# Kernel optimization log

Measured on AMD Instinct MI355X. Metric: run time of the kernel, lower is better.

The kernel has to match this reference:

```python
import jax, jax.numpy as jnp
import numpy as np
from jax import lax

B, E, V, T = 16384, 256, 128, 16
TAU = 1.0


def _gru(x, h, Wih, Whh, bih, bhh):
    # torch.nn.GRUCell math
    gi = x @ Wih.T + bih
    gh = h @ Whh.T + bhh
    ir, iz, i_n = jnp.split(gi, 3, axis=-1)
    hr, hz, h_n = jnp.split(gh, 3, axis=-1)
    r = jax.nn.sigmoid(ir + hr)
    z = jax.nn.sigmoid(iz + hz)
    n = jnp.tanh(i_n + r * h_n)
    return (1.0 - z) * n + z * h


def setup_inputs() -> dict:
    key = jax.random.key(0)
    ks = jax.random.split(key, 10)
    s = 0.05
    w = lambda k, shape: jax.random.normal(k, shape, jnp.float32) * s
    return {
        "x": jax.random.normal(ks[0], (B, E), jnp.float32),
        "global_idxes": jnp.arange(B, dtype=jnp.int32),
        "uniform_noise": jax.random.uniform(ks[1], (T, B, V), dtype=jnp.float32),
        "dec_Wd2e": w(ks[2], (E, V)), "dec_bd2e": jnp.zeros((E,), jnp.float32),
        "dec_Wih": w(ks[3], (3 * E, E)), "dec_Whh": w(ks[4], (3 * E, E)),
        "dec_bih": jnp.zeros((3 * E,), jnp.float32), "dec_bhh": jnp.zeros((3 * E,), jnp.float32),
        "dec_We2d": w(ks[5], (V, E)), "dec_be2d": jnp.zeros((V,), jnp.float32),
        "enc_Wd2e": w(ks[6], (E, V)), "enc_bd2e": jnp.zeros((E,), jnp.float32),
        "enc_Wih": w(ks[7], (3 * E, E)), "enc_Whh": w(ks[8], (3 * E, E)),
        "enc_bih": jnp.zeros((3 * E,), jnp.float32), "enc_bhh": jnp.zeros((3 * E,), jnp.float32),
    }


def _forward(x, uniform_noise,
             dec_Wd2e, dec_bd2e, dec_Wih, dec_Whh, dec_bih, dec_bhh, dec_We2d, dec_be2d,
             enc_Wd2e, enc_bd2e, enc_Wih, enc_Whh, enc_bih, enc_bhh):
    Bn = x.shape[0]
    # gumbel noise from pre-sampled uniforms (deterministic)
    gnoise = -jnp.log(-jnp.log(uniform_noise + 1e-10) + 1e-10)  # [T,B,V]

    # ---- GumbelDecoder: sequential GRUCell decode with alive/dead masking ----
    def dec_step(carry, g_t):
        state, last_tok, alive, N, t = carry
        emb = last_tok @ dec_Wd2e.T + dec_bd2e
        state = _gru(emb, state, dec_Wih, dec_Whh, dec_bih, dec_bhh)
        logits = state @ dec_We2d.T + dec_be2d
        y_soft = jax.nn.softmax((logits + g_t) / TAU, axis=-1)
        idx = jnp.argmax(y_soft, axis=-1)
        y_hard = jax.nn.one_hot(idx, V, dtype=y_soft.dtype)
        # straight-through hard gumbel-softmax
        y = y_soft + lax.stop_gradient(y_hard - y_soft)
        ended = idx == 0  # token 0 is the terminator
        N = jnp.where(ended, jnp.minimum(N, t), N)
        alive = alive & (~ended)
        # dead rows (incl. newly ended) have their token zeroed, as in torch
        y = jnp.where(alive[:, None], y, 0.0)
        return (state, y, alive, N, t + 1), y

    init = (x, jnp.zeros((Bn, V), x.dtype), jnp.ones((Bn,), bool),
            jnp.full((Bn,), T, jnp.int32), jnp.int32(0))
    (_, _, _, N, _), utt = lax.scan(dec_step, init, gnoise)  # utt: [T,B,V]

    # ---- OnehotEncoder: sequential GRUCell encode with alive sieve (masked) ----
    def enc_step(carry, u_t):
        state, out_state, alive = carry
        emb = u_t @ enc_Wd2e.T + enc_bd2e
        state = _gru(emb, state, enc_Wih, enc_Whh, enc_bih, enc_bhh)
        out_state = jnp.where(alive[:, None], state, out_state)
        ended = u_t[:, 0] > 0.5  # terminator seen in utterance
        alive = alive & (~ended)
        return (state, out_state, alive), None

    z0 = jnp.zeros((Bn, E), x.dtype)
    (_, reconst, _), _ = lax.scan(enc_step, (z0, z0, jnp.ones((Bn,), bool)), utt)

    utterance = jnp.transpose(utt, (1, 0, 2))  # [B,T,V]
    return utterance, N, reconst


def reference(x, global_idxes, uniform_noise,
              dec_Wd2e, dec_bd2e, dec_Wih, dec_Whh, dec_bih, dec_bhh, dec_We2d, dec_be2d,
              enc_Wd2e, enc_bd2e, enc_Wih, enc_Whh, enc_bih, enc_bhh):
    del global_idxes  # unused by the original forward
    return _forward(x, uniform_noise,
                    dec_Wd2e, dec_bd2e, dec_Wih, dec_Whh, dec_bih, dec_bhh, dec_We2d, dec_be2d,
                    enc_Wd2e, enc_bd2e, enc_Wih, enc_Whh, enc_bih, enc_bhh)
```

## Files before the change

kernel.cpp:

```cpp
#include <hip/hip_runtime.h>


namespace {
constexpr int kB  = 16384;
constexpr int kE  = 256;
constexpr int kV  = 128;
constexpr int kT  = 16;
constexpr int kG3 = 768;
constexpr int kR  = 16;

constexpr int kOffWdhhT  = 0;
constexpr int kOffWehhT  = kG3 * kE;
constexpr int kOffWe2dT  = 2 * kG3 * kE;
constexpr int kOffDecTab = kOffWe2dT + kV * kE;
constexpr int kOffEncTab = kOffDecTab + 129 * kG3;
}

__device__ __forceinline__ float sigmf(float v) { return 1.0f / (1.0f + expf(-v)); }
__device__ __forceinline__ float gumbelf(float u) {
  return -logf(-logf(u + 1e-10f) + 1e-10f);
}

__global__ void prep_transpose(const float* __restrict__ dWhh,
                               const float* __restrict__ eWhh,
                               const float* __restrict__ We2d,
                               float* __restrict__ ws) {
  const int n1 = kG3 * kE;
  const int n2 = n1 + kG3 * kE;
  const int n3 = n2 + kV * kE;
  for (int i = blockIdx.x * blockDim.x + threadIdx.x; i < n3;
       i += gridDim.x * blockDim.x) {
    if (i < n1) {
      const int k = i / kG3, j = i - k * kG3;
      ws[i] = dWhh[j * kE + k];
    } else if (i < n2) {
      const int t = i - n1;
      const int k = t / kG3, j = t - k * kG3;
      ws[i] = eWhh[j * kE + k];
    } else {
      const int t = i - n2;
      const int k = t / kV, v = t - k * kV;
      ws[i] = We2d[v * kE + k];
    }
  }
}

__global__ void prep_tables(const float* __restrict__ Wih,
                            const float* __restrict__ Wd2e,
                            const float* __restrict__ bd2e,
                            const float* __restrict__ bih,
                            float* __restrict__ tab) {
  const int i = blockIdx.x * blockDim.x + threadIdx.x;
  if (i >= 129 * kG3) return;
  const int v = i / kG3, j = i - v * kG3;
  const float* wr = Wih + j * kE;
  float acc = 0.0f;
  if (v < kV) {
    for (int k = 0; k < kE; ++k) acc = fmaf(wr[k], Wd2e[k * kV + v] + bd2e[k], acc);
  } else {
    for (int k = 0; k < kE; ++k) acc = fmaf(wr[k], bd2e[k], acc);
  }
  tab[i] = acc + bih[j];
}

__device__ __forceinline__ void mv16(float acc[kR][3], const float (*h)[kR],
                                     const float* __restrict__ WT, const int u) {
#pragma unroll
  for (int r = 0; r < kR; ++r) { acc[r][0] = 0.f; acc[r][1] = 0.f; acc[r][2] = 0.f; }
  const float* wp = WT + u;
#pragma unroll 2
  for (int k = 0; k < kE; ++k) {
    const float4 hA = *(const float4*)(&h[k][0]);
    const float4 hB = *(const float4*)(&h[k][4]);
    const float4 hC = *(const float4*)(&h[k][8]);
    const float4 hD = *(const float4*)(&h[k][12]);
    const float w0 = wp[0], w1 = wp[kE], w2 = wp[2 * kE];
    wp += kG3;
    const float hv[kR] = {hA.x, hA.y, hA.z, hA.w, hB.x, hB.y, hB.z, hB.w,
                          hC.x, hC.y, hC.z, hC.w, hD.x, hD.y, hD.z, hD.w};
#pragma unroll
    for (int r = 0; r < kR; ++r) {
      acc[r][0] = fmaf(hv[r], w0, acc[r][0]);
      acc[r][1] = fmaf(hv[r], w1, acc[r][1]);
      acc[r][2] = fmaf(hv[r], w2, acc[r][2]);
    }
  }
}

__device__ __forceinline__ void pw16(const float acc[kR][3], float (*h)[kR],
                                     const float* __restrict__ Tab,
                                     const int* toks,
                                     const float br, const float bz,
                                     const float bn, const int u) {
  const float4 o0 = *(const float4*)(&h[u][0]);
  const float4 o1 = *(const float4*)(&h[u][4]);
  const float4 o2 = *(const float4*)(&h[u][8]);
  const float4 o3 = *(const float4*)(&h[u][12]);
  const float ho[kR] = {o0.x, o0.y, o0.z, o0.w, o1.x, o1.y, o1.z, o1.w,
                        o2.x, o2.y, o2.z, o2.w, o3.x, o3.y, o3.z, o3.w};
  float hn[kR];
#pragma unroll
  for (int r = 0; r < kR; ++r) {
    const float* gp = Tab + toks[r] * kG3 + u;
    const float gr = gp[0], gz = gp[kE], gn = gp[2 * kE];
    const float rg = sigmf(gr + acc[r][0] + br);
    const float zg = sigmf(gz + acc[r][1] + bz);
    const float ng = tanhf(gn + rg * (acc[r][2] + bn));
    hn[r] = (1.0f - zg) * ng + zg * ho[r];
  }
  *(float4*)(&h[u][0])  = make_float4(hn[0], hn[1], hn[2], hn[3]);
  *(float4*)(&h[u][4])  = make_float4(hn[4], hn[5], hn[6], hn[7]);
  *(float4*)(&h[u][8])  = make_float4(hn[8], hn[9], hn[10], hn[11]);
  *(float4*)(&h[u][12]) = make_float4(hn[12], hn[13], hn[14], hn[15]);
}

__launch_bounds__(256, 4)
__global__ void gumbel_fused(const float* __restrict__ x,
                             const float* __restrict__ unoise,
                             const float* __restrict__ dbhh,
                             const float* __restrict__ dbe2d,
                             const float* __restrict__ ebhh,
                             const float* __restrict__ ws,
                             float* __restrict__ out) {
  const float* WdhhT  = ws + kOffWdhhT;
  const float* WehhT  = ws + kOffWehhT;
  const float* We2dT  = ws + kOffWe2dT;
  const float* DecTab = ws + kOffDecTab;
  const float* EncTab = ws + kOffEncTab;

  __shared__ float hd[kE][kR];
  __shared__ float he[kE][kR];
  __shared__ int   tok_sh[kR];

  const int tid  = (int)threadIdx.x;
  const int w    = tid >> 6;
  const int jx   = tid & 63;
  const int row0 = (int)blockIdx.x * kR;
  const int u    = tid;

  for (int i = tid; i < kR * kE; i += 256) {
    const int r = i >> 8, k = i & (kE - 1);
    hd[k][r] = x[(size_t)(row0 + r) * kE + k];
    he[k][r] = 0.0f;
  }
  if (tid < kR) tok_sh[tid] = kV;
  __syncthreads();

  float Nn[4];
  bool alive[4];
#pragma unroll
  for (int q = 0; q < 4; ++q) { Nn[q] = (float)kT; alive[q] = true; }

  const float dbr = dbhh[u], dbz = dbhh[kE + u], dbn = dbhh[2 * kE + u];
  const float ebr = ebhh[u], ebz = ebhh[kE + u], ebn = ebhh[2 * kE + u];
  const float2 be2 = *(const float2*)(dbe2d + 2 * jx);

  float acc[kR][3];

  for (int t = 0; t < kT; ++t) {
    mv16(acc, hd, WdhhT, u);
    __syncthreads();
    pw16(acc, hd, DecTab, tok_sh, dbr, dbz, dbn, u);
    __syncthreads();

    mv16(acc, he, WehhT, u);

    {
      float l0[4] = {0.f, 0.f, 0.f, 0.f}, l1[4] = {0.f, 0.f, 0.f, 0.f};
      const float* wp2 = We2dT + 2 * jx;
#pragma unroll 2
      for (int k = 0; k < kE; ++k) {
        const float2 wv = *(const float2*)wp2;
        wp2 += kV;
        const float4 hq = *(const float4*)(&hd[k][4 * w]);
        const float hv[4] = {hq.x, hq.y, hq.z, hq.w};
#pragma unroll
        for (int q = 0; q < 4; ++q) {
          l0[q] = fmaf(hv[q], wv.x, l0[q]);
          l1[q] = fmaf(hv[q], wv.y, l1[q]);
        }
      }
      const size_t rbase = (size_t)row0 + 4 * w;
#pragma unroll
      for (int q = 0; q < 4; ++q) {
        const float2 uu =
            *(const float2*)(unoise + ((size_t)t * kB + rbase + q) * kV + 2 * jx);
        const float a0 = l0[q] + be2.x + gumbelf(uu.x);
        const float a1 = l1[q] + be2.y + gumbelf(uu.y);
        float mv; int mi;
        if (a1 > a0) { mv = a1; mi = 2 * jx + 1; } else { mv = a0; mi = 2 * jx; }
#pragma unroll
        for (int off = 32; off >= 1; off >>= 1) {
          const float ov = __shfl_xor(mv, off, 64);
          const int   oi = __shfl_xor(mi, off, 64);
          if (ov > mv || (ov == mv && oi < mi)) { mv = ov; mi = oi; }
        }
        const bool ended = (mi == 0);
        if (ended) Nn[q] = fminf(Nn[q], (float)t);
        const bool anew = alive[q] && !ended;
        alive[q] = anew;
        if (jx == 0) tok_sh[4 * w + q] = anew ? mi : kV;
        float2 pr;
        pr.x = (anew && mi == 2 * jx) ? 1.0f : 0.0f;
        pr.y = (anew && mi == 2 * jx + 1) ? 1.0f : 0.0f;
        *reinterpret_cast<float2*>(out + ((rbase + q) * kT + t) * kV + 2 * jx) = pr;
      }
    }
    __syncthreads();
    pw16(acc, he, EncTab, tok_sh, ebr, ebz, ebn, u);
    __syncthreads();
  }

  const size_t uttN = (size_t)kB * kT * kV;
  if (jx == 0) {
#pragma unroll
    for (int q = 0; q < 4; ++q) out[uttN + row0 + 4 * w + q] = Nn[q];
  }
  for (int i = tid; i < kR * kE; i += 256) {
    const int r = i >> 8, k = i & (kE - 1);
    out[uttN + kB + (size_t)(row0 + r) * kE + k] = he[k][r];
  }
}

extern "C" void kernel_launch(void* const* d_in, const int* in_sizes, int n_in,
                              void* d_out, int out_size, void* d_ws, size_t ws_size,
                              hipStream_t stream) {
  (void)in_sizes; (void)n_in; (void)out_size; (void)ws_size;
  const float* x      = (const float*)d_in[0];
  const float* unoise = (const float*)d_in[2];
  const float* dWd2e  = (const float*)d_in[3];
  const float* dbd2e  = (const float*)d_in[4];
  const float* dWih   = (const float*)d_in[5];
  const float* dWhh   = (const float*)d_in[6];
  const float* dbih   = (const float*)d_in[7];
  const float* dbhh   = (const float*)d_in[8];
  const float* dWe2d  = (const float*)d_in[9];
  const float* dbe2d  = (const float*)d_in[10];
  const float* eWd2e  = (const float*)d_in[11];
  const float* ebd2e  = (const float*)d_in[12];
  const float* eWih   = (const float*)d_in[13];
  const float* eWhh   = (const float*)d_in[14];
  const float* ebih   = (const float*)d_in[15];
  const float* ebhh   = (const float*)d_in[16];
  float* ws = (float*)d_ws;

  prep_transpose<<<1664, 256, 0, stream>>>(dWhh, eWhh, dWe2d, ws);
  prep_tables<<<(129 * kG3 + 255) / 256, 256, 0, stream>>>(
      dWih, dWd2e, dbd2e, dbih, ws + kOffDecTab);
  prep_tables<<<(129 * kG3 + 255) / 256, 256, 0, stream>>>(
      eWih, eWd2e, ebd2e, ebih, ws + kOffEncTab);
  gumbel_fused<<<kB / kR, 256, 0, stream>>>(
      x, unoise, dbhh, dbe2d, ebhh, ws, (float*)d_out);
}
```

Measured before the change: 4.151 ms.

## Split fused decode/encode into separate kernels with 64-row blocks and token workspace

Splits the single fused decoder+encoder kernel into a decoder kernel and an encoder kernel that communicate through a per-timestep token array in workspace. Each block now processes 64 rows with 1024 threads, and each thread computes 16 hidden units for one row using float4 weight loads and a scalar h read from LDS. This gives more reuse of each weight load across rows. The r/z parts of bhh are folded into the precomputed input tables. The changes add an extra kernel launch and global token traffic, and raise LDS use per block (64 KB) and register pressure from 48 accumulators, which may limit occupancy.

```diff
diff --git a/kernel.cpp b/kernel.cpp
--- a/kernel.cpp
+++ b/kernel.cpp
@@ -7,13 +7,13 @@
 constexpr int kV  = 128;
 constexpr int kT  = 16;
 constexpr int kG3 = 768;
-constexpr int kR  = 16;
 
 constexpr int kOffWdhhT  = 0;
 constexpr int kOffWehhT  = kG3 * kE;
 constexpr int kOffWe2dT  = 2 * kG3 * kE;
 constexpr int kOffDecTab = kOffWe2dT + kV * kE;
 constexpr int kOffEncTab = kOffDecTab + 129 * kG3;
+constexpr int kOffTok    = kOffEncTab + 129 * kG3;
 }
 
 __device__ __forceinline__ float sigmf(float v) { return 1.0f / (1.0f + expf(-v)); }
@@ -49,6 +49,7 @@
                             const float* __restrict__ Wd2e,
                             const float* __restrict__ bd2e,
                             const float* __restrict__ bih,
+                            const float* __restrict__ bhh,
                             float* __restrict__ tab) {
   const int i = blockIdx.x * blockDim.x + threadIdx.x;
   if (i >= 129 * kG3) return;
@@ -60,154 +61,143 @@
   } else {
     for (int k = 0; k < kE; ++k) acc = fmaf(wr[k], bd2e[k], acc);
   }
-  tab[i] = acc + bih[j];
-}
-
-__device__ __forceinline__ void mv16(float acc[kR][3], const float (*h)[kR],
-                                     const float* __restrict__ WT, const int u) {
-#pragma unroll
-  for (int r = 0; r < kR; ++r) { acc[r][0] = 0.f; acc[r][1] = 0.f; acc[r][2] = 0.f; }
-  const float* wp = WT + u;
-#pragma unroll 2
+  tab[i] = acc + bih[j] + (j < 2 * kE ? bhh[j] : 0.0f);
+}
+
+__device__ __forceinline__ void mv64(float acc[16][3],
+                                     const float* __restrict__ hbuf,
+                                     const float* __restrict__ WT,
+                                     const int u0, const int jx) {
+#pragma unroll
+  for (int j = 0; j < 16; ++j) { acc[j][0] = 0.f; acc[j][1] = 0.f; acc[j][2] = 0.f; }
+  const float* wk = WT + u0;
   for (int k = 0; k < kE; ++k) {
-    const float4 hA = *(const float4*)(&h[k][0]);
-    const float4 hB = *(const float4*)(&h[k][4]);
-    const float4 hC = *(const float4*)(&h[k][8]);
-    const float4 hD = *(const float4*)(&h[k][12]);
-    const float w0 = wp[0], w1 = wp[kE], w2 = wp[2 * kE];
-    wp += kG3;
-    const float hv[kR] = {hA.x, hA.y, hA.z, hA.w, hB.x, hB.y, hB.z, hB.w,
-                          hC.x, hC.y, hC.z, hC.w, hD.x, hD.y, hD.z, hD.w};
-#pragma unroll
-    for (int r = 0; r < kR; ++r) {
-      acc[r][0] = fmaf(hv[r], w0, acc[r][0]);
-      acc[r][1] = fmaf(hv[r], w1, acc[r][1]);
-      acc[r][2] = fmaf(hv[r], w2, acc[r][2]);
-    }
-  }
-}
-
-__device__ __forceinline__ void pw16(const float acc[kR][3], float (*h)[kR],
+    const float hk = hbuf[k * 64 + jx];
+    const float4 a0 = *(const float4*)(wk + 0);
+    const float4 a1 = *(const float4*)(wk + 4);
+    const float4 a2 = *(const float4*)(wk + 8);
+    const float4 a3 = *(const float4*)(wk + 12);
+    const float4 b0 = *(const float4*)(wk + kE + 0);
+    const float4 b1 = *(const float4*)(wk + kE + 4);
+    const float4 b2 = *(const float4*)(wk + kE + 8);
+    const float4 b3 = *(const float4*)(wk + kE + 12);
+    const float4 c0 = *(const float4*)(wk + 2 * kE + 0);
+    const float4 c1 = *(const float4*)(wk + 2 * kE + 4);
+    const float4 c2 = *(const float4*)(wk + 2 * kE + 8);
+    const float4 c3 = *(const float4*)(wk + 2 * kE + 12);
+    const float wa[16] = {a0.x, a0.y, a0.z, a0.w, a1.x, a1.y, a1.z, a1.w,
+                          a2.x, a2.y, a2.z, a2.w, a3.x, a3.y, a3.z, a3.w};
+    const float wb[16] = {b0.x, b0.y, b0.z, b0.w, b1.x, b1.y, b1.z, b1.w,
+                          b2.x, b2.y, b2.z, b2.w, b3.x, b3.y, b3.z, b3.w};
+    const float wc[16] = {c0.x, c0.y, c0.z, c0.w, c1.x, c1.y, c1.z, c1.w,
+                          c2.x, c2.y, c2.z, c2.w, c3.x, c3.y, c3.z, c3.w};
+#pragma unroll
+    for (int j = 0; j < 16; ++j) {
+      acc[j][0] = fmaf(hk, wa[j], acc[j][0]);
+      acc[j][1] = fmaf(hk, wb[j], acc[j][1]);
+      acc[j][2] = fmaf(hk, wc[j], acc[j][2]);
+    }
+    wk += kG3;
+  }
+}
+
+__device__ __forceinline__ void pw64(const float acc[16][3],
+                                     float* __restrict__ hbuf,
                                      const float* __restrict__ Tab,
-                                     const int* toks,
-                                     const float br, const float bz,
-                                     const float bn, const int u) {
-  const float4 o0 = *(const float4*)(&h[u][0]);
-  const float4 o1 = *(const float4*)(&h[u][4]);
-  const float4 o2 = *(const float4*)(&h[u][8]);
-  const float4 o3 = *(const float4*)(&h[u][12]);
-  const float ho[kR] = {o0.x, o0.y, o0.z, o0.w, o1.x, o1.y, o1.z, o1.w,
-                        o2.x, o2.y, o2.z, o2.w, o3.x, o3.y, o3.z, o3.w};
-  float hn[kR];
-#pragma unroll
-  for (int r = 0; r < kR; ++r) {
-    const float* gp = Tab + toks[r] * kG3 + u;
-    const float gr = gp[0], gz = gp[kE], gn = gp[2 * kE];
-    const float rg = sigmf(gr + acc[r][0] + br);
-    const float zg = sigmf(gz + acc[r][1] + bz);
-    const float ng = tanhf(gn + rg * (acc[r][2] + bn));
-    hn[r] = (1.0f - zg) * ng + zg * ho[r];
-  }
-  *(float4*)(&h[u][0])  = make_float4(hn[0], hn[1], hn[2], hn[3]);
-  *(float4*)(&h[u][4])  = make_float4(hn[4], hn[5], hn[6], hn[7]);
-  *(float4*)(&h[u][8])  = make_float4(hn[8], hn[9], hn[10], hn[11]);
-  *(float4*)(&h[u][12]) = make_float4(hn[12], hn[13], hn[14], hn[15]);
-}
-
-__launch_bounds__(256, 4)
-__global__ void gumbel_fused(const float* __restrict__ x,
-                             const float* __restrict__ unoise,
-                             const float* __restrict__ dbhh,
-                             const float* __restrict__ dbe2d,
-                             const float* __restrict__ ebhh,
-                             const float* __restrict__ ws,
-                             float* __restrict__ out) {
-  const float* WdhhT  = ws + kOffWdhhT;
-  const float* WehhT  = ws + kOffWehhT;
-  const float* We2dT  = ws + kOffWe2dT;
-  const float* DecTab = ws + kOffDecTab;
-  const float* EncTab = ws + kOffEncTab;
-
-  __shared__ float hd[kE][kR];
-  __shared__ float he[kE][kR];
-  __shared__ int   tok_sh[kR];
+                                     const float* __restrict__ bhh,
+                                     const int tk, const int u0, const int jx) {
+  const float* gp = Tab + tk * kG3 + u0;
+#pragma unroll
+  for (int j = 0; j < 16; ++j) {
+    const float gr = gp[j], gz = gp[kE + j], gn = gp[2 * kE + j];
+    const float bn = bhh[2 * kE + u0 + j];
+    const float ho = hbuf[(u0 + j) * 64 + jx];
+    const float rg = sigmf(gr + acc[j][0]);
+    const float zg = sigmf(gz + acc[j][1]);
+    const float ng = tanhf(gn + rg * (acc[j][2] + bn));
+    hbuf[(u0 + j) * 64 + jx] = (1.0f - zg) * ng + zg * ho;
+  }
+}
+
+__launch_bounds__(1024, 4)
+__global__ void dec_kernel(const float* __restrict__ x,
+                           const float* __restrict__ unoise,
+                           const float* __restrict__ dbhh,
+                           const float* __restrict__ dbe2d,
+                           const float* __restrict__ ws,
+                           int* __restrict__ tokws,
+                           float* __restrict__ out) {
+  const float* WT  = ws + kOffWdhhT;
+  const float* W2T = ws + kOffWe2dT;
+  const float* Tab = ws + kOffDecTab;
+  __shared__ float hd[kE * 64];
 
   const int tid  = (int)threadIdx.x;
   const int w    = tid >> 6;
   const int jx   = tid & 63;
-  const int row0 = (int)blockIdx.x * kR;
-  const int u    = tid;
-
-  for (int i = tid; i < kR * kE; i += 256) {
+  const int row0 = (int)blockIdx.x * 64;
+  const int u0   = __builtin_amdgcn_readfirstlane(w * 16);
+
+  for (int i = tid; i < 64 * kE; i += 1024) {
     const int r = i >> 8, k = i & (kE - 1);
-    hd[k][r] = x[(size_t)(row0 + r) * kE + k];
-    he[k][r] = 0.0f;
-  }
-  if (tid < kR) tok_sh[tid] = kV;
+    hd[k * 64 + r] = x[(size_t)(row0 + r) * kE + k];
+  }
+  if (tid < 64) tokws[row0 + tid] = kV;
   __syncthreads();
 
   float Nn[4];
   bool alive[4];
 #pragma unroll
   for (int q = 0; q < 4; ++q) { Nn[q] = (float)kT; alive[q] = true; }
-
-  const float dbr = dbhh[u], dbz = dbhh[kE + u], dbn = dbhh[2 * kE + u];
-  const float ebr = ebhh[u], ebz = ebhh[kE + u], ebn = ebhh[2 * kE + u];
   const float2 be2 = *(const float2*)(dbe2d + 2 * jx);
 
-  float acc[kR][3];
-
+  float acc[16][3];
   for (int t = 0; t < kT; ++t) {
-    mv16(acc, hd, WdhhT, u);
-    __syncthreads();
-    pw16(acc, hd, DecTab, tok_sh, dbr, dbz, dbn, u);
-    __syncthreads();
-
-    mv16(acc, he, WehhT, u);
-
-    {
-      float l0[4] = {0.f, 0.f, 0.f, 0.f}, l1[4] = {0.f, 0.f, 0.f, 0.f};
-      const float* wp2 = We2dT + 2 * jx;
+    mv64(acc, hd, WT, u0, jx);
+    __syncthreads();
+    const int tk = tokws[t * kB + row0 + jx];
+    pw64(acc, hd, Tab, dbhh, tk, u0, jx);
+    __syncthreads();
+
+    float l0[4] = {0.f, 0.f, 0.f, 0.f}, l1[4] = {0.f, 0.f, 0.f, 0.f};
+    const float* wp2 = W2T + 2 * jx;
 #pragma unroll 2
-      for (int k = 0; k < kE; ++k) {
-        const float2 wv = *(const float2*)wp2;
-        wp2 += kV;
-        const float4 hq = *(const float4*)(&hd[k][4 * w]);
-        const float hv[4] = {hq.x, hq.y, hq.z, hq.w};
-#pragma unroll
-        for (int q = 0; q < 4; ++q) {
-          l0[q] = fmaf(hv[q], wv.x, l0[q]);
-          l1[q] = fmaf(hv[q], wv.y, l1[q]);
-        }
+    for (int k = 0; k < kE; ++k) {
+      const float4 hq = *(const float4*)(&hd[k * 64 + 4 * w]);
+      const float2 wv = *(const float2*)wp2;
+      wp2 += kV;
+      const float hv[4] = {hq.x, hq.y, hq.z, hq.w};
+#pragma unroll
+      for (int q = 0; q < 4; ++q) {
+        l0[q] = fmaf(hv[q], wv.x, l0[q]);
+        l1[q] = fmaf(hv[q], wv.y, l1[q]);
       }
-      const size_t rbase = (size_t)row0 + 4 * w;
-#pragma unroll
-      for (int q = 0; q < 4; ++q) {
-        const float2 uu =
-            *(const float2*)(unoise + ((size_t)t * kB + rbase + q) * kV + 2 * jx);
-        const float a0 = l0[q] + be2.x + gumbelf(uu.x);
-        const float a1 = l1[q] + be2.y + gumbelf(uu.y);
-        float mv; int mi;
-        if (a1 > a0) { mv = a1; mi = 2 * jx + 1; } else { mv = a0; mi = 2 * jx; }
-#pragma unroll
-        for (int off = 32; off >= 1; off >>= 1) {
-          const float ov = __shfl_xor(mv, off, 64);
-          const int   oi = __shfl_xor(mi, off, 64);
-          if (ov > mv || (ov == mv && oi < mi)) { mv = ov; mi = oi; }
-        }
-        const bool ended = (mi == 0);
-        if (ended) Nn[q] = fminf(Nn[q], (float)t);
-        const bool anew = alive[q] && !ended;
-        alive[q] = anew;
-        if (jx == 0) tok_sh[4 * w + q] = anew ? mi : kV;
-        float2 pr;
-        pr.x = (anew && mi == 2 * jx) ? 1.0f : 0.0f;
-        pr.y = (anew && mi == 2 * jx + 1) ? 1.0f : 0.0f;
-        *reinterpret_cast<float2*>(out + ((rbase + q) * kT + t) * kV + 2 * jx) = pr;
+    }
+    const size_t rbase = (size_t)row0 + 4 * w;
+#pragma unroll
+    for (int q = 0; q < 4; ++q) {
+      const float2 uu =
+          *(const float2*)(unoise + ((size_t)t * kB + rbase + q) * kV + 2 * jx);
+      const float a0 = l0[q] + be2.x + gumbelf(uu.x);
+      const float a1 = l1[q] + be2.y + gumbelf(uu.y);
+      float mv; int mi;
+      if (a1 > a0) { mv = a1; mi = 2 * jx + 1; } else { mv = a0; mi = 2 * jx; }
+#pragma unroll
+      for (int off = 32; off >= 1; off >>= 1) {
+        const float ov = __shfl_xor(mv, off, 64);
+        const int   oi = __shfl_xor(mi, off, 64);
+        if (ov > mv || (ov == mv && oi < mi)) { mv = ov; mi = oi; }
       }
-    }
-    __syncthreads();
-    pw16(acc, he, EncTab, tok_sh, ebr, ebz, ebn, u);
+      const bool ended = (mi == 0);
+      if (ended) Nn[q] = fminf(Nn[q], (float)t);
+      const bool anew = alive[q] && !ended;
+      alive[q] = anew;
+      if (jx == 0) tokws[(t + 1) * kB + rbase + q] = anew ? mi : kV;
+      float2 pr;
+      pr.x = (anew && mi == 2 * jx) ? 1.0f : 0.0f;
+      pr.y = (anew && mi == 2 * jx + 1) ? 1.0f : 0.0f;
+      *reinterpret_cast<float2*>(out + ((rbase + q) * kT + t) * kV + 2 * jx) = pr;
+    }
     __syncthreads();
   }
 
@@ -216,9 +206,39 @@
 #pragma unroll
     for (int q = 0; q < 4; ++q) out[uttN + row0 + 4 * w + q] = Nn[q];
   }
-  for (int i = tid; i < kR * kE; i += 256) {
+}
+
+__launch_bounds__(1024, 4)
+__global__ void enc_kernel(const float* __restrict__ ebhh,
+                           const float* __restrict__ ws,
+                           const int* __restrict__ tokws,
+                           float* __restrict__ out) {
+  const float* WT  = ws + kOffWehhT;
+  const float* Tab = ws + kOffEncTab;
+  __shared__ float he[kE * 64];
+
+  const int tid  = (int)threadIdx.x;
+  const int w    = tid >> 6;
+  const int jx   = tid & 63;
+  const int row0 = (int)blockIdx.x * 64;
+  const int u0   = __builtin_amdgcn_readfirstlane(w * 16);
+
+  for (int i = tid; i < 64 * kE; i += 1024) he[i] = 0.0f;
+  __syncthreads();
+
+  float acc[16][3];
+  for (int t = 0; t < kT; ++t) {
+    mv64(acc, he, WT, u0, jx);
+    __syncthreads();
+    const int tk = tokws[(t + 1) * kB + row0 + jx];
+    pw64(acc, he, Tab, ebhh, tk, u0, jx);
+    __syncthreads();
+  }
+
+  const size_t base = (size_t)kB * kT * kV + kB;
+  for (int i = tid; i < 64 * kE; i += 1024) {
     const int r = i >> 8, k = i & (kE - 1);
-    out[uttN + kB + (size_t)(row0 + r) * kE + k] = he[k][r];
+    out[base + (size_t)(row0 + r) * kE + k] = he[k * 64 + r];
   }
 }
 
@@ -242,13 +262,16 @@
   const float* eWhh   = (const float*)d_in[14];
   const float* ebih   = (const float*)d_in[15];
   const float* ebhh   = (const float*)d_in[16];
-  float* ws = (float*)d_ws;
+  float* ws   = (float*)d_ws;
+  int* tokws  = (int*)(ws + kOffTok);
 
   prep_transpose<<<1664, 256, 0, stream>>>(dWhh, eWhh, dWe2d, ws);
   prep_tables<<<(129 * kG3 + 255) / 256, 256, 0, stream>>>(
-      dWih, dWd2e, dbd2e, dbih, ws + kOffDecTab);
+      dWih, dWd2e, dbd2e, dbih, dbhh, ws + kOffDecTab);
   prep_tables<<<(129 * kG3 + 255) / 256, 256, 0, stream>>>(
-      eWih, eWd2e, ebd2e, ebih, ws + kOffEncTab);
-  gumbel_fused<<<kB / kR, 256, 0, stream>>>(
-      x, unoise, dbhh, dbe2d, ebhh, ws, (float*)d_out);
-}
+      eWih, eWd2e, ebd2e, ebih, ebhh, ws + kOffEncTab);
+  dec_kernel<<<kB / 64, 1024, 0, stream>>>(
+      x, unoise, dbhh, dbe2d, ws, tokws, (float*)d_out);
+  enc_kernel<<<kB / 64, 1024, 0, stream>>>(
+      ebhh, ws, tokws, (float*)d_out);
+}
```

Measured after the change: 5.314 ms. 1.28x slower.
